# Optimization experiments

Measured on AMD Instinct MI355X. Metric: run time of the kernel, lower is better.

## Reference

```python
import jax, jax.numpy as jnp
from jax import lax
import numpy as np

K = 11          # NUM_TAGS
S = K + 2       # with start/stop
START, STOP = K, K + 1
O_TAG = 0
B, T = 4096, 1024
NEG = -10000.0


def setup_inputs() -> dict:
    key = jax.random.key(0)
    k1, k2, k3 = jax.random.split(key, 3)
    e = jax.random.normal(k1, (B, T, K), dtype=jnp.float32)
    Tmat = jax.random.normal(k2, (S, S), dtype=jnp.float32) * 0.1
    Tmat = Tmat.at[:, START].set(NEG)
    Tmat = Tmat.at[STOP, :].set(NEG)
    Tmat = Tmat.at[O_TAG, O_TAG].add(-2.0)
    tags = jax.random.randint(k3, (B, T), 0, K, dtype=jnp.int32)
    mask = jnp.ones((B, T), dtype=bool)
    return {"e": e, "Tmat": Tmat, "tags": tags, "mask": mask}


def _nll(e, Tmat, tags, mask):
    maskf = mask.astype(e.dtype)
    # ---- forward algorithm (log partition) via scan over time ----
    a0 = jnp.full((e.shape[0], S), NEG, dtype=e.dtype).at[:, START].set(0.0)

    def step(a, inp):
        e_t, m_t = inp                                   # (B,K), (B,)
        # scores[b, to] = lse_from(a[b, from] + Tmat[from, to])
        sc = jax.nn.logsumexp(a[:, :, None] + Tmat[None, :, :], axis=1)  # (B,S)
        sc = sc.at[:, :K].add(e_t)
        a = jnp.where(m_t[:, None], sc, a)
        return a, None

    a, _ = lax.scan(step, a0, (jnp.swapaxes(e, 0, 1), jnp.swapaxes(mask, 0, 1)))
    logZ = jax.nn.logsumexp(a[:, :K] + Tmat[:K, STOP][None, :], axis=1)  # (B,)

    # ---- gold path score (fully vectorized) ----
    tg = jnp.clip(tags, 0, K - 1)
    em = jnp.take_along_axis(e, tg[:, :, None], axis=2)[..., 0] * maskf  # (B,T)
    trans = Tmat[tg[:, :-1], tg[:, 1:]] * maskf[:, 1:]                   # (B,T-1)
    last = mask.astype(jnp.int32).sum(1) - 1                             # (B,)
    last_tag = jnp.take_along_axis(tg, last[:, None], axis=1)[:, 0]
    gold = Tmat[START, tg[:, 0]] + em.sum(1) + trans.sum(1) + Tmat[last_tag, STOP]

    return jnp.mean(logZ - gold)


def reference(e, Tmat, tags, mask):
    return _nll(e, Tmat, tags, mask)
```

## Files before the change

kernel.cpp:

```cpp
#include <hip/hip_runtime.h>

#define KTAGS 11
#define SS    13
#define TT    1024
#define BB    4096
#define GPW   4
#define UNR   16

__global__ __launch_bounds__(64)
void crf_scan_kernel(const float* __restrict__ e,
                     const float* __restrict__ Tmat,
                     const int*   __restrict__ tags,
                     float*       __restrict__ out_per_b)
{
    __shared__ float sT[SS * SS];
    const int tid = threadIdx.x;
    for (int i = tid; i < SS * SS; i += 64) sT[i] = Tmat[i];

    const int g   = tid >> 4;
    const int to  = tid & 15;
    const int toT = (to < SS) ? to : (SS - 1);
    const int toE = (to < KTAGS) ? to : (KTAGS - 1);
    const int b   = blockIdx.x * GPW + g;

    __syncthreads();

    float W[16];
#pragma unroll
    for (int r = 0; r < 16; ++r) {
        const int f = (to - r) & 15;
        W[r] = (f < KTAGS && to <= SS - 1 && to != KTAGS)
                 ? __expf(sT[f * SS + toT]) : 0.f;
        if (to >= SS) W[r] = 0.f;
    }
    const float eTstop = __expf(sT[toT * SS + (SS - 1)]);

    const float* pe  = e    + (size_t)b * TT * KTAGS + toE;
    const int*   tgp = tags + (size_t)b * TT;

    const float e0  = pe[0];
    const int   tg0 = tgp[0];
    float aP = (to < SS) ? __expf(sT[(SS - 2) * SS + toT] + e0) : 0.f;

    float cacc   = 0.f;
    float em_acc = (to == tg0) ? e0 : 0.f;

    float ebuf[UNR];
    int   tbuf[UNR];
#pragma unroll
    for (int j = 0; j < UNR; ++j) {
        ebuf[j] = pe[(size_t)(1 + j) * KTAGS];
        tbuf[j] = tgp[1 + j];
    }

    float scP = 1.f, eeP = 0.f;

#define STEP(J, E_T, TG)                                                       \
    {                                                                          \
        const float X_T = __expf(E_T);         \
        float ac0, ac1, ac2, ac3;                                              \
        asm volatile(                                                          \
          "s_nop 1\n\t"                                                        \
          "v_mul_f32 %0, %4, %5\n\t"                                           \
          "v_mul_f32_dpp %1, %4, %6  row_ror:1  row_mask:0xf bank_mask:0xf\n\t"\
          "v_mul_f32_dpp %2, %4, %7  row_ror:2  row_mask:0xf bank_mask:0xf\n\t"\
          "v_mul_f32_dpp %3, %4, %8  row_ror:3  row_mask:0xf bank_mask:0xf\n\t"\
          "v_fmac_f32_dpp %0, %4, %9  row_ror:4  row_mask:0xf bank_mask:0xf\n\t"\
          "v_fmac_f32_dpp %1, %4, %10 row_ror:5  row_mask:0xf bank_mask:0xf\n\t"\
          "v_fmac_f32_dpp %2, %4, %11 row_ror:6  row_mask:0xf bank_mask:0xf\n\t"\
          "v_fmac_f32_dpp %3, %4, %12 row_ror:7  row_mask:0xf bank_mask:0xf\n\t"\
          "v_fmac_f32_dpp %0, %4, %13 row_ror:8  row_mask:0xf bank_mask:0xf\n\t"\
          "v_fmac_f32_dpp %1, %4, %14 row_ror:9  row_mask:0xf bank_mask:0xf\n\t"\
          "v_fmac_f32_dpp %2, %4, %15 row_ror:10 row_mask:0xf bank_mask:0xf\n\t"\
          "v_fmac_f32_dpp %3, %4, %16 row_ror:11 row_mask:0xf bank_mask:0xf\n\t"\
          "v_fmac_f32_dpp %0, %4, %17 row_ror:12 row_mask:0xf bank_mask:0xf\n\t"\
          "v_fmac_f32_dpp %1, %4, %18 row_ror:13 row_mask:0xf bank_mask:0xf\n\t"\
          "v_fmac_f32_dpp %2, %4, %19 row_ror:14 row_mask:0xf bank_mask:0xf\n\t"\
          "v_fmac_f32_dpp %3, %4, %20 row_ror:15 row_mask:0xf bank_mask:0xf\n\t"\
          : "=&v"(ac0), "=&v"(ac1), "=&v"(ac2), "=&v"(ac3)                     \
          : "v"(aP), "v"(W[0]), "v"(W[1]), "v"(W[2]),  "v"(W[3]),              \
            "v"(W[4]), "v"(W[5]), "v"(W[6]),  "v"(W[7]), "v"(W[8]),            \
            "v"(W[9]), "v"(W[10]), "v"(W[11]), "v"(W[12]), "v"(W[13]),         \
            "v"(W[14]), "v"(W[15]));                                           \
        float xsc = X_T;                                                       \
        if (((J) & 7) == 0) { cacc += eeP * 0.6931471805599453f; xsc *= scP; } \
        aP = ((ac0 + ac1) + (ac2 + ac3)) * xsc;                                \
        if (((J) & 7) == 7) {    \
            float mm;                                                          \
            asm volatile(                                                      \
              "s_nop 1\n\t"                                                    \
              "v_max_f32_dpp %0, %1, %1 row_ror:8 row_mask:0xf bank_mask:0xf\n\t"\
              "s_nop 1\n\t"                                                    \
              "v_max_f32_dpp %0, %0, %0 row_ror:4 row_mask:0xf bank_mask:0xf\n\t"\
              "s_nop 1\n\t"                                                    \
              "v_max_f32_dpp %0, %0, %0 quad_perm:[1,0,3,2] row_mask:0xf bank_mask:0xf\n\t"\
              "s_nop 1\n\t"                                                    \
              "v_max_f32_dpp %0, %0, %0 quad_perm:[2,3,0,1] row_mask:0xf bank_mask:0xf\n\t"\
              : "=&v"(mm) : "v"(aP));                                          \
            const int ee = (int)((__float_as_uint(mm) >> 23) & 0xFFu) - 127;   \
            scP = __uint_as_float((unsigned)(127 - ee) << 23);                 \
            eeP = (float)ee;                                                   \
        }                                                                      \
        em_acc += (to == (TG)) ? (E_T) : 0.f;                                  \
    }

    const float* qe = pe  + (size_t)(1 + UNR) * KTAGS;
    const int*   qt = tgp + 1 + UNR;

    for (int tb = 1; tb + 2 * UNR <= TT; tb += UNR) {
#pragma unroll
        for (int j = 0; j < UNR; ++j) {
            const float E_T = ebuf[j];
            const int   TG  = tbuf[j];
            ebuf[j] = qe[j * KTAGS];
            tbuf[j] = qt[j];
            STEP(j, E_T, TG)
        }
        qe += (size_t)UNR * KTAGS; qt += UNR;
    }

#pragma unroll
    for (int j = 0; j < UNR; ++j) {
        const float E_T = ebuf[j];
        const int   TG  = tbuf[j];
        if (j < UNR - 1) {
            ebuf[j] = qe[j * KTAGS];
            tbuf[j] = qt[j];
        }
        STEP(j, E_T, TG)
    }

#pragma unroll
    for (int j = 0; j < UNR - 1; ++j) {
        STEP(j, ebuf[j], tbuf[j])
    }
#undef STEP

    float z  = (to < KTAGS) ? aP * eTstop : 0.f;
    float em = em_acc;
#pragma unroll
    for (int s = 8; s >= 1; s >>= 1) {
        z  += __shfl_xor(z,  s, 16);
        em += __shfl_xor(em, s, 16);
    }
    if (to == 0) {
        const float logZ = cacc + __logf(z);
        out_per_b[b] = logZ - em;
    }
}

__global__ __launch_bounds__(64)
void gold_kernel(const float* __restrict__ Tmat,
                 const int*   __restrict__ tags,
                 float*       __restrict__ out_per_b)
{
    __shared__ float sT[SS * SS];
    __shared__ int   stg[TT];
    const int tid = threadIdx.x;
    const int b   = blockIdx.x;

    for (int i = tid; i < SS * SS; i += 64) sT[i] = Tmat[i];
    const int4* tg4 = (const int4*)(tags + (size_t)b * TT);
    int4* s4 = (int4*)stg;
#pragma unroll
    for (int k = 0; k < TT / 4 / 64; ++k) s4[tid + 64 * k] = tg4[tid + 64 * k];
    __syncthreads();

    float s = 0.f;
    const int t0 = tid * 16;
#pragma unroll
    for (int k = 1; k <= 16; ++k) {
        const int t = t0 + k;
        if (t < TT) s += sT[stg[t - 1] * SS + stg[t]];
    }
    if (tid == 0) {
        s += sT[(SS - 2) * SS + stg[0]];
        s += sT[stg[TT - 1] * SS + (SS - 1)];
    }
#pragma unroll
    for (int d = 32; d >= 1; d >>= 1) s += __shfl_xor(s, d, 64);
    if (tid == 0) out_per_b[b] -= s;
}

__global__ __launch_bounds__(256)
void reduce_mean_kernel(const float* __restrict__ v, float* __restrict__ out, int n)
{
    __shared__ double sbuf[256];
    double s = 0.0;
    for (int i = threadIdx.x; i < n; i += 256) s += (double)v[i];
    sbuf[threadIdx.x] = s;
    __syncthreads();
    for (int k = 128; k > 0; k >>= 1) {
        if ((int)threadIdx.x < k) sbuf[threadIdx.x] += sbuf[threadIdx.x + k];
        __syncthreads();
    }
    if (threadIdx.x == 0) out[0] = (float)(sbuf[0] / (double)n);
}

extern "C" void kernel_launch(void* const* d_in, const int* in_sizes, int n_in,
                              void* d_out, int out_size, void* d_ws, size_t ws_size,
                              hipStream_t stream)
{
    const float* e    = (const float*)d_in[0];
    const float* Tmat = (const float*)d_in[1];
    const int*   tags = (const int*)d_in[2];

    float* ws  = (float*)d_ws;
    float* out = (float*)d_out;

    crf_scan_kernel<<<BB / GPW, 64, 0, stream>>>(e, Tmat, tags, ws);
    gold_kernel<<<BB, 64, 0, stream>>>(Tmat, tags, ws);
    reduce_mean_kernel<<<1, 256, 0, stream>>>(ws, out, BB);
}
```

Baseline: 96.87 us.

## Split CRF forward scan into forward and backward halves meeting at midpoint

Runs the sequential forward recursion over the first half of the sequence and a backward recursion over the second half in separate blocks, doubling the number of independent waves and halving the serial chain length. A new combine kernel computes logZ from the dot product of forward and backward vectors at the midpoint, in double precision. It keeps a fallback to the original single-direction scan when the workspace is too small. It adds an extra kernel launch and workspace traffic.

```diff
diff --git a/kernel.cpp b/kernel.cpp
--- a/kernel.cpp
+++ b/kernel.cpp
@@ -6,59 +6,18 @@
 #define BB    4096
 #define GPW   4
 #define UNR   16
-
-__global__ __launch_bounds__(64)
-void crf_scan_kernel(const float* __restrict__ e,
-                     const float* __restrict__ Tmat,
-                     const int*   __restrict__ tags,
-                     float*       __restrict__ out_per_b)
-{
-    __shared__ float sT[SS * SS];
-    const int tid = threadIdx.x;
-    for (int i = tid; i < SS * SS; i += 64) sT[i] = Tmat[i];
-
-    const int g   = tid >> 4;
-    const int to  = tid & 15;
-    const int toT = (to < SS) ? to : (SS - 1);
-    const int toE = (to < KTAGS) ? to : (KTAGS - 1);
-    const int b   = blockIdx.x * GPW + g;
-
-    __syncthreads();
-
-    float W[16];
-#pragma unroll
-    for (int r = 0; r < 16; ++r) {
-        const int f = (to - r) & 15;
-        W[r] = (f < KTAGS && to <= SS - 1 && to != KTAGS)
-                 ? __expf(sT[f * SS + toT]) : 0.f;
-        if (to >= SS) W[r] = 0.f;
-    }
-    const float eTstop = __expf(sT[toT * SS + (SS - 1)]);
-
-    const float* pe  = e    + (size_t)b * TT * KTAGS + toE;
-    const int*   tgp = tags + (size_t)b * TT;
-
-    const float e0  = pe[0];
-    const int   tg0 = tgp[0];
-    float aP = (to < SS) ? __expf(sT[(SS - 2) * SS + toT] + e0) : 0.f;
-
-    float cacc   = 0.f;
-    float em_acc = (to == tg0) ? e0 : 0.f;
-
-    float ebuf[UNR];
-    int   tbuf[UNR];
-#pragma unroll
-    for (int j = 0; j < UNR; ++j) {
-        ebuf[j] = pe[(size_t)(1 + j) * KTAGS];
-        tbuf[j] = tgp[1 + j];
-    }
-
-    float scP = 1.f, eeP = 0.f;
-
-#define STEP(J, E_T, TG)                                                       \
-    {                                                                          \
-        const float X_T = __expf(E_T);         \
-        float ac0, ac1, ac2, ac3;                                              \
+#define HALF  512
+
+#define WS_VA   0
+#define WS_UB   (11*BB)
+#define WS_CF   (22*BB)
+#define WS_EF   (23*BB)
+#define WS_CB   (24*BB)
+#define WS_EB   (25*BB)
+#define WS_NLL  (26*BB)
+#define WS_FLOATS (27*BB)
+
+#define ROTSUM(A0,A1,A2,A3,SRC)                                                \
         asm volatile(                                                          \
           "s_nop 1\n\t"                                                        \
           "v_mul_f32 %0, %4, %5\n\t"                                           \
@@ -77,26 +36,35 @@
           "v_fmac_f32_dpp %1, %4, %18 row_ror:13 row_mask:0xf bank_mask:0xf\n\t"\
           "v_fmac_f32_dpp %2, %4, %19 row_ror:14 row_mask:0xf bank_mask:0xf\n\t"\
           "v_fmac_f32_dpp %3, %4, %20 row_ror:15 row_mask:0xf bank_mask:0xf\n\t"\
-          : "=&v"(ac0), "=&v"(ac1), "=&v"(ac2), "=&v"(ac3)                     \
-          : "v"(aP), "v"(W[0]), "v"(W[1]), "v"(W[2]),  "v"(W[3]),              \
+          : "=&v"(A0), "=&v"(A1), "=&v"(A2), "=&v"(A3)                         \
+          : "v"(SRC), "v"(W[0]), "v"(W[1]), "v"(W[2]),  "v"(W[3]),             \
             "v"(W[4]), "v"(W[5]), "v"(W[6]),  "v"(W[7]), "v"(W[8]),            \
             "v"(W[9]), "v"(W[10]), "v"(W[11]), "v"(W[12]), "v"(W[13]),         \
-            "v"(W[14]), "v"(W[15]));                                           \
+            "v"(W[14]), "v"(W[15]))
+
+#define MAXRED(MM, SRC)                                                        \
+        asm volatile(                                                          \
+          "s_nop 1\n\t"                                                        \
+          "v_max_f32_dpp %0, %1, %1 row_ror:8 row_mask:0xf bank_mask:0xf\n\t"  \
+          "s_nop 1\n\t"                                                        \
+          "v_max_f32_dpp %0, %0, %0 row_ror:4 row_mask:0xf bank_mask:0xf\n\t"  \
+          "s_nop 1\n\t"                                                        \
+          "v_max_f32_dpp %0, %0, %0 quad_perm:[1,0,3,2] row_mask:0xf bank_mask:0xf\n\t"\
+          "s_nop 1\n\t"                                                        \
+          "v_max_f32_dpp %0, %0, %0 quad_perm:[2,3,0,1] row_mask:0xf bank_mask:0xf\n\t"\
+          : "=&v"(MM) : "v"(SRC))
+
+#define STEP(J, E_T, TG)                                                       \
+    {                                                                          \
+        const float X_T = __expf(E_T);                                         \
+        float ac0, ac1, ac2, ac3;                                              \
+        ROTSUM(ac0, ac1, ac2, ac3, aP);                                        \
         float xsc = X_T;                                                       \
         if (((J) & 7) == 0) { cacc += eeP * 0.6931471805599453f; xsc *= scP; } \
         aP = ((ac0 + ac1) + (ac2 + ac3)) * xsc;                                \
-        if (((J) & 7) == 7) {    \
+        if (((J) & 7) == 7) {                                                  \
             float mm;                                                          \
-            asm volatile(                                                      \
-              "s_nop 1\n\t"                                                    \
-              "v_max_f32_dpp %0, %1, %1 row_ror:8 row_mask:0xf bank_mask:0xf\n\t"\
-              "s_nop 1\n\t"                                                    \
-              "v_max_f32_dpp %0, %0, %0 row_ror:4 row_mask:0xf bank_mask:0xf\n\t"\
-              "s_nop 1\n\t"                                                    \
-              "v_max_f32_dpp %0, %0, %0 quad_perm:[1,0,3,2] row_mask:0xf bank_mask:0xf\n\t"\
-              "s_nop 1\n\t"                                                    \
-              "v_max_f32_dpp %0, %0, %0 quad_perm:[2,3,0,1] row_mask:0xf bank_mask:0xf\n\t"\
-              : "=&v"(mm) : "v"(aP));                                          \
+            MAXRED(mm, aP);                                                    \
             const int ee = (int)((__float_as_uint(mm) >> 23) & 0xFFu) - 127;   \
             scP = __uint_as_float((unsigned)(127 - ee) << 23);                 \
             eeP = (float)ee;                                                   \
@@ -104,9 +72,224 @@
         em_acc += (to == (TG)) ? (E_T) : 0.f;                                  \
     }
 
+template<int DIR>
+__device__ __forceinline__ void scan_dir(const float* __restrict__ e,
+                                         const int*   __restrict__ tags,
+                                         const float* sT,
+                                         float*       __restrict__ ws,
+                                         int b, int to)
+{
+    const int toT = (to < SS) ? to : (SS - 1);
+    const int toE = (to < KTAGS) ? to : (KTAGS - 1);
+
+    float W[16];
+#pragma unroll
+    for (int r = 0; r < 16; ++r) {
+        const int f = (to - r) & 15;
+        if (DIR > 0) {
+            W[r] = (f < KTAGS && to <= SS - 1 && to != KTAGS)
+                     ? __expf(sT[f * SS + toT]) : 0.f;
+            if (to >= SS) W[r] = 0.f;
+        } else {
+            W[r] = (to < KTAGS && f < KTAGS) ? __expf(sT[to * SS + f]) : 0.f;
+        }
+    }
+
+    const float* ebase = e    + (size_t)b * TT * KTAGS + toE;
+    const int*   tbase = tags + (size_t)b * TT;
+
+    float aP, em_acc, cacc = 0.f;
+    if (DIR > 0) {
+        const float E0 = ebase[0];
+        const int   tg0 = tbase[0];
+        aP = (to < SS) ? __expf(sT[(SS - 2) * SS + toT] + E0) : 0.f;
+        em_acc = (to == tg0) ? E0 : 0.f;
+    } else {
+        const float E0 = ebase[(size_t)(TT - 1) * KTAGS];
+        const int   tg0 = tbase[TT - 1];
+        aP = (to < KTAGS) ? __expf(E0 + sT[toT * SS + (SS - 1)]) : 0.f;
+        em_acc = (to == tg0) ? E0 : 0.f;
+    }
+
+    const ptrdiff_t estep = (ptrdiff_t)DIR * KTAGS;
+    const float* peU = ebase + ((DIR > 0) ? (ptrdiff_t)KTAGS : (ptrdiff_t)(TT - 2) * KTAGS);
+    const int*   tgU = tbase + ((DIR > 0) ? 1 : (TT - 2));
+
+    float ebuf[UNR]; int tbuf[UNR];
+#pragma unroll
+    for (int j = 0; j < UNR; ++j) {
+        ebuf[j] = peU[estep * j];
+        tbuf[j] = tgU[DIR * j];
+    }
+
+    float scP = 1.f, eeP = 0.f;
+    const float* qe = peU + estep * UNR;
+    const int*   qt = tgU + DIR * UNR;
+
+    for (int tb = 0; tb + 2 * UNR <= (HALF - 1); tb += UNR) {
+#pragma unroll
+        for (int j = 0; j < UNR; ++j) {
+            const float E_T = ebuf[j];
+            const int   TG  = tbuf[j];
+            ebuf[j] = qe[estep * j];
+            tbuf[j] = qt[DIR * j];
+            STEP(j, E_T, TG)
+        }
+        qe += estep * UNR; qt += DIR * UNR;
+    }
+#pragma unroll
+    for (int j = 0; j < UNR; ++j) {
+        const float E_T = ebuf[j];
+        const int   TG  = tbuf[j];
+        if (j < UNR - 1) { ebuf[j] = qe[estep * j]; tbuf[j] = qt[DIR * j]; }
+        STEP(j, E_T, TG)
+    }
+#pragma unroll
+    for (int j = 0; j < UNR - 1; ++j) {
+        STEP(j, ebuf[j], tbuf[j])
+    }
+
+    float em = em_acc;
+#pragma unroll
+    for (int s = 8; s >= 1; s >>= 1) em += __shfl_xor(em, s, 16);
+
+    if (DIR > 0) {
+        float ac0, ac1, ac2, ac3;
+        ROTSUM(ac0, ac1, ac2, ac3, aP);
+        const float v = (ac0 + ac1) + (ac2 + ac3);
+        if (to < KTAGS) ws[WS_VA + to * BB + b] = v;
+        if (to == 0) { ws[WS_CF + b] = cacc; ws[WS_EF + b] = em; }
+    } else {
+        if (to < KTAGS) ws[WS_UB + to * BB + b] = aP;
+        if (to == 0) { ws[WS_CB + b] = cacc; ws[WS_EB + b] = em; }
+    }
+}
+
+__global__ __launch_bounds__(64)
+void crf_scan2_kernel(const float* __restrict__ e,
+                      const float* __restrict__ Tmat,
+                      const int*   __restrict__ tags,
+                      float*       __restrict__ ws)
+{
+    __shared__ float sT[SS * SS];
+    const int tid = threadIdx.x;
+    for (int i = tid; i < SS * SS; i += 64) sT[i] = Tmat[i];
+    __syncthreads();
+
+    const int g  = tid >> 4;
+    const int to = tid & 15;
+    const int b  = ((int)blockIdx.x & (BB / GPW - 1)) * GPW + g;
+
+    if ((int)blockIdx.x < BB / GPW) scan_dir<+1>(e, tags, sT, ws, b, to);
+    else                            scan_dir<-1>(e, tags, sT, ws, b, to);
+}
+
+__global__ __launch_bounds__(256)
+void combine_kernel(float* __restrict__ ws)
+{
+    const int b = blockIdx.x * 256 + threadIdx.x;
+    double dot = 0.0;
+#pragma unroll
+    for (int s = 0; s < KTAGS; ++s)
+        dot += (double)ws[WS_VA + s * BB + b] * (double)ws[WS_UB + s * BB + b];
+    const float logZ = (float)((double)ws[WS_CF + b] + (double)ws[WS_CB + b] + log(dot));
+    ws[WS_NLL + b] = logZ - ws[WS_EF + b] - ws[WS_EB + b];
+}
+
+__global__ __launch_bounds__(64)
+void gold_kernel(const float* __restrict__ Tmat,
+                 const int*   __restrict__ tags,
+                 float*       __restrict__ nll)
+{
+    __shared__ float sT[SS * SS];
+    __shared__ int   stg[TT];
+    const int tid = threadIdx.x;
+    const int b   = blockIdx.x;
+
+    for (int i = tid; i < SS * SS; i += 64) sT[i] = Tmat[i];
+    const int4* tg4 = (const int4*)(tags + (size_t)b * TT);
+    int4* s4 = (int4*)stg;
+#pragma unroll
+    for (int k = 0; k < TT / 4 / 64; ++k) s4[tid + 64 * k] = tg4[tid + 64 * k];
+    __syncthreads();
+
+    float s = 0.f;
+    const int t0 = tid * 16;
+#pragma unroll
+    for (int k = 1; k <= 16; ++k) {
+        const int t = t0 + k;
+        if (t < TT) s += sT[stg[t - 1] * SS + stg[t]];
+    }
+    if (tid == 0) {
+        s += sT[(SS - 2) * SS + stg[0]];
+        s += sT[stg[TT - 1] * SS + (SS - 1)];
+    }
+#pragma unroll
+    for (int d = 32; d >= 1; d >>= 1) s += __shfl_xor(s, d, 64);
+    if (tid == 0) nll[b] -= s;
+}
+
+__global__ __launch_bounds__(256)
+void reduce_mean_kernel(const float* __restrict__ v, float* __restrict__ out, int n)
+{
+    __shared__ double sbuf[256];
+    double s = 0.0;
+    for (int i = threadIdx.x; i < n; i += 256) s += (double)v[i];
+    sbuf[threadIdx.x] = s;
+    __syncthreads();
+    for (int k = 128; k > 0; k >>= 1) {
+        if ((int)threadIdx.x < k) sbuf[threadIdx.x] += sbuf[threadIdx.x + k];
+        __syncthreads();
+    }
+    if (threadIdx.x == 0) out[0] = (float)(sbuf[0] / (double)n);
+}
+
+__global__ __launch_bounds__(64)
+void crf_scan_full_kernel(const float* __restrict__ e,
+                          const float* __restrict__ Tmat,
+                          const int*   __restrict__ tags,
+                          float*       __restrict__ out_per_b)
+{
+    __shared__ float sT[SS * SS];
+    const int tid = threadIdx.x;
+    for (int i = tid; i < SS * SS; i += 64) sT[i] = Tmat[i];
+
+    const int g   = tid >> 4;
+    const int to  = tid & 15;
+    const int toT = (to < SS) ? to : (SS - 1);
+    const int toE = (to < KTAGS) ? to : (KTAGS - 1);
+    const int b   = blockIdx.x * GPW + g;
+    __syncthreads();
+
+    float W[16];
+#pragma unroll
+    for (int r = 0; r < 16; ++r) {
+        const int f = (to - r) & 15;
+        W[r] = (f < KTAGS && to <= SS - 1 && to != KTAGS)
+                 ? __expf(sT[f * SS + toT]) : 0.f;
+        if (to >= SS) W[r] = 0.f;
+    }
+    const float eTstop = __expf(sT[toT * SS + (SS - 1)]);
+
+    const float* pe  = e    + (size_t)b * TT * KTAGS + toE;
+    const int*   tgp = tags + (size_t)b * TT;
+
+    const float e0  = pe[0];
+    const int   tg0 = tgp[0];
+    float aP = (to < SS) ? __expf(sT[(SS - 2) * SS + toT] + e0) : 0.f;
+    float cacc = 0.f;
+    float em_acc = (to == tg0) ? e0 : 0.f;
+
+    float ebuf[UNR]; int tbuf[UNR];
+#pragma unroll
+    for (int j = 0; j < UNR; ++j) {
+        ebuf[j] = pe[(size_t)(1 + j) * KTAGS];
+        tbuf[j] = tgp[1 + j];
+    }
+    float scP = 1.f, eeP = 0.f;
+
     const float* qe = pe  + (size_t)(1 + UNR) * KTAGS;
     const int*   qt = tgp + 1 + UNR;
-
     for (int tb = 1; tb + 2 * UNR <= TT; tb += UNR) {
 #pragma unroll
         for (int j = 0; j < UNR; ++j) {
@@ -118,23 +301,17 @@
         }
         qe += (size_t)UNR * KTAGS; qt += UNR;
     }
-
 #pragma unroll
     for (int j = 0; j < UNR; ++j) {
         const float E_T = ebuf[j];
         const int   TG  = tbuf[j];
-        if (j < UNR - 1) {
-            ebuf[j] = qe[j * KTAGS];
-            tbuf[j] = qt[j];
-        }
+        if (j < UNR - 1) { ebuf[j] = qe[j * KTAGS]; tbuf[j] = qt[j]; }
         STEP(j, E_T, TG)
     }
-
 #pragma unroll
     for (int j = 0; j < UNR - 1; ++j) {
         STEP(j, ebuf[j], tbuf[j])
     }
-#undef STEP
 
     float z  = (to < KTAGS) ? aP * eTstop : 0.f;
     float em = em_acc;
@@ -149,54 +326,6 @@
     }
 }
 
-__global__ __launch_bounds__(64)
-void gold_kernel(const float* __restrict__ Tmat,
-                 const int*   __restrict__ tags,
-                 float*       __restrict__ out_per_b)
-{
-    __shared__ float sT[SS * SS];
-    __shared__ int   stg[TT];
-    const int tid = threadIdx.x;
-    const int b   = blockIdx.x;
-
-    for (int i = tid; i < SS * SS; i += 64) sT[i] = Tmat[i];
-    const int4* tg4 = (const int4*)(tags + (size_t)b * TT);
-    int4* s4 = (int4*)stg;
-#pragma unroll
-    for (int k = 0; k < TT / 4 / 64; ++k) s4[tid + 64 * k] = tg4[tid + 64 * k];
-    __syncthreads();
-
-    float s = 0.f;
-    const int t0 = tid * 16;
-#pragma unroll
-    for (int k = 1; k <= 16; ++k) {
-        const int t = t0 + k;
-        if (t < TT) s += sT[stg[t - 1] * SS + stg[t]];
-    }
-    if (tid == 0) {
-        s += sT[(SS - 2) * SS + stg[0]];
-        s += sT[stg[TT - 1] * SS + (SS - 1)];
-    }
-#pragma unroll
-    for (int d = 32; d >= 1; d >>= 1) s += __shfl_xor(s, d, 64);
-    if (tid == 0) out_per_b[b] -= s;
-}
-
-__global__ __launch_bounds__(256)
-void reduce_mean_kernel(const float* __restrict__ v, float* __restrict__ out, int n)
-{
-    __shared__ double sbuf[256];
-    double s = 0.0;
-    for (int i = threadIdx.x; i < n; i += 256) s += (double)v[i];
-    sbuf[threadIdx.x] = s;
-    __syncthreads();
-    for (int k = 128; k > 0; k >>= 1) {
-        if ((int)threadIdx.x < k) sbuf[threadIdx.x] += sbuf[threadIdx.x + k];
-        __syncthreads();
-    }
-    if (threadIdx.x == 0) out[0] = (float)(sbuf[0] / (double)n);
-}
-
 extern "C" void kernel_launch(void* const* d_in, const int* in_sizes, int n_in,
                               void* d_out, int out_size, void* d_ws, size_t ws_size,
                               hipStream_t stream)
@@ -208,7 +337,14 @@
     float* ws  = (float*)d_ws;
     float* out = (float*)d_out;
 
-    crf_scan_kernel<<<BB / GPW, 64, 0, stream>>>(e, Tmat, tags, ws);
-    gold_kernel<<<BB, 64, 0, stream>>>(Tmat, tags, ws);
-    reduce_mean_kernel<<<1, 256, 0, stream>>>(ws, out, BB);
-}
+    if (ws_size >= (size_t)WS_FLOATS * sizeof(float)) {
+        crf_scan2_kernel<<<2 * BB / GPW, 64, 0, stream>>>(e, Tmat, tags, ws);
+        combine_kernel<<<BB / 256, 256, 0, stream>>>(ws);
+        gold_kernel<<<BB, 64, 0, stream>>>(Tmat, tags, ws + WS_NLL);
+        reduce_mean_kernel<<<1, 256, 0, stream>>>(ws + WS_NLL, out, BB);
+    } else {
+        crf_scan_full_kernel<<<BB / GPW, 64, 0, stream>>>(e, Tmat, tags, ws);
+        gold_kernel<<<BB, 64, 0, stream>>>(Tmat, tags, ws);
+        reduce_mean_kernel<<<1, 256, 0, stream>>>(ws, out, BB);
+    }
+}
```

After: 80.51 us. -16.9%, faster.

## Split CRF forward scan into forward and backward halves meeting midway

Applied to the files above, without the earlier changes.

Replaces the single sequential forward recursion with two interleaved chains per sequence: a forward alpha chain from the start and a backward beta chain from the end, each covering half the timesteps. The two results are combined with one extra matrix-vector step and a double-precision dot product. This halves the serial dependency length and gives the scheduler two independent DPP chains to interleave, hiding instruction latency. The cost is twice the register use for weights and buffers, which may lower occupancy, plus reverse-direction loads for the backward chain.

```diff
diff --git a/kernel.cpp b/kernel.cpp
--- a/kernel.cpp
+++ b/kernel.cpp
@@ -5,60 +5,71 @@
 #define TT    1024
 #define BB    4096
 #define GPW   4
-#define UNR   16
-
-__global__ __launch_bounds__(64)
-void crf_scan_kernel(const float* __restrict__ e,
-                     const float* __restrict__ Tmat,
-                     const int*   __restrict__ tags,
-                     float*       __restrict__ out_per_b)
-{
-    __shared__ float sT[SS * SS];
-    const int tid = threadIdx.x;
-    for (int i = tid; i < SS * SS; i += 64) sT[i] = Tmat[i];
-
-    const int g   = tid >> 4;
-    const int to  = tid & 15;
-    const int toT = (to < SS) ? to : (SS - 1);
-    const int toE = (to < KTAGS) ? to : (KTAGS - 1);
-    const int b   = blockIdx.x * GPW + g;
-
-    __syncthreads();
-
-    float W[16];
-#pragma unroll
-    for (int r = 0; r < 16; ++r) {
-        const int f = (to - r) & 15;
-        W[r] = (f < KTAGS && to <= SS - 1 && to != KTAGS)
-                 ? __expf(sT[f * SS + toT]) : 0.f;
-        if (to >= SS) W[r] = 0.f;
-    }
-    const float eTstop = __expf(sT[toT * SS + (SS - 1)]);
-
-    const float* pe  = e    + (size_t)b * TT * KTAGS + toE;
-    const int*   tgp = tags + (size_t)b * TT;
-
-    const float e0  = pe[0];
-    const int   tg0 = tgp[0];
-    float aP = (to < SS) ? __expf(sT[(SS - 2) * SS + toT] + e0) : 0.f;
-
-    float cacc   = 0.f;
-    float em_acc = (to == tg0) ? e0 : 0.f;
-
-    float ebuf[UNR];
-    int   tbuf[UNR];
-#pragma unroll
-    for (int j = 0; j < UNR; ++j) {
-        ebuf[j] = pe[(size_t)(1 + j) * KTAGS];
-        tbuf[j] = tgp[1 + j];
-    }
-
-    float scP = 1.f, eeP = 0.f;
-
-#define STEP(J, E_T, TG)                                                       \
-    {                                                                          \
-        const float X_T = __expf(E_T);         \
-        float ac0, ac1, ac2, ac3;                                              \
+#define UNR   8
+#define LN2   0.6931471805599453f
+
+#define ROTSUM2(A0,A1,A2,A3,B0,B1,B2,B3,SA,SB,WA,WB)                           \
+        asm volatile(                                                          \
+          "s_nop 1\n\t"                                                        \
+          "v_mul_f32 %0, %8, %10\n\t"                                          \
+          "v_mul_f32_dpp %1, %8, %11 row_ror:1  row_mask:0xf bank_mask:0xf\n\t"\
+          "v_mul_f32_dpp %2, %8, %12 row_ror:2  row_mask:0xf bank_mask:0xf\n\t"\
+          "v_mul_f32_dpp %3, %8, %13 row_ror:3  row_mask:0xf bank_mask:0xf\n\t"\
+          "v_mul_f32 %4, %9, %26\n\t"                                          \
+          "v_mul_f32_dpp %5, %9, %27 row_ror:1  row_mask:0xf bank_mask:0xf\n\t"\
+          "v_mul_f32_dpp %6, %9, %28 row_ror:2  row_mask:0xf bank_mask:0xf\n\t"\
+          "v_mul_f32_dpp %7, %9, %29 row_ror:3  row_mask:0xf bank_mask:0xf\n\t"\
+          "v_fmac_f32_dpp %0, %8, %14 row_ror:4  row_mask:0xf bank_mask:0xf\n\t"\
+          "v_fmac_f32_dpp %4, %9, %30 row_ror:4  row_mask:0xf bank_mask:0xf\n\t"\
+          "v_fmac_f32_dpp %1, %8, %15 row_ror:5  row_mask:0xf bank_mask:0xf\n\t"\
+          "v_fmac_f32_dpp %5, %9, %31 row_ror:5  row_mask:0xf bank_mask:0xf\n\t"\
+          "v_fmac_f32_dpp %2, %8, %16 row_ror:6  row_mask:0xf bank_mask:0xf\n\t"\
+          "v_fmac_f32_dpp %6, %9, %32 row_ror:6  row_mask:0xf bank_mask:0xf\n\t"\
+          "v_fmac_f32_dpp %3, %8, %17 row_ror:7  row_mask:0xf bank_mask:0xf\n\t"\
+          "v_fmac_f32_dpp %7, %9, %33 row_ror:7  row_mask:0xf bank_mask:0xf\n\t"\
+          "v_fmac_f32_dpp %0, %8, %18 row_ror:8  row_mask:0xf bank_mask:0xf\n\t"\
+          "v_fmac_f32_dpp %4, %9, %34 row_ror:8  row_mask:0xf bank_mask:0xf\n\t"\
+          "v_fmac_f32_dpp %1, %8, %19 row_ror:9  row_mask:0xf bank_mask:0xf\n\t"\
+          "v_fmac_f32_dpp %5, %9, %35 row_ror:9  row_mask:0xf bank_mask:0xf\n\t"\
+          "v_fmac_f32_dpp %2, %8, %20 row_ror:10 row_mask:0xf bank_mask:0xf\n\t"\
+          "v_fmac_f32_dpp %6, %9, %36 row_ror:10 row_mask:0xf bank_mask:0xf\n\t"\
+          "v_fmac_f32_dpp %3, %8, %21 row_ror:11 row_mask:0xf bank_mask:0xf\n\t"\
+          "v_fmac_f32_dpp %7, %9, %37 row_ror:11 row_mask:0xf bank_mask:0xf\n\t"\
+          "v_fmac_f32_dpp %0, %8, %22 row_ror:12 row_mask:0xf bank_mask:0xf\n\t"\
+          "v_fmac_f32_dpp %4, %9, %38 row_ror:12 row_mask:0xf bank_mask:0xf\n\t"\
+          "v_fmac_f32_dpp %1, %8, %23 row_ror:13 row_mask:0xf bank_mask:0xf\n\t"\
+          "v_fmac_f32_dpp %5, %9, %39 row_ror:13 row_mask:0xf bank_mask:0xf\n\t"\
+          "v_fmac_f32_dpp %2, %8, %24 row_ror:14 row_mask:0xf bank_mask:0xf\n\t"\
+          "v_fmac_f32_dpp %6, %9, %40 row_ror:14 row_mask:0xf bank_mask:0xf\n\t"\
+          "v_fmac_f32_dpp %3, %8, %25 row_ror:15 row_mask:0xf bank_mask:0xf\n\t"\
+          "v_fmac_f32_dpp %7, %9, %41 row_ror:15 row_mask:0xf bank_mask:0xf\n\t"\
+          : "=&v"(A0), "=&v"(A1), "=&v"(A2), "=&v"(A3),                        \
+            "=&v"(B0), "=&v"(B1), "=&v"(B2), "=&v"(B3)                         \
+          : "v"(SA), "v"(SB),                                                  \
+            "v"(WA[0]),"v"(WA[1]),"v"(WA[2]),"v"(WA[3]),"v"(WA[4]),"v"(WA[5]), \
+            "v"(WA[6]),"v"(WA[7]),"v"(WA[8]),"v"(WA[9]),"v"(WA[10]),"v"(WA[11]),\
+            "v"(WA[12]),"v"(WA[13]),"v"(WA[14]),"v"(WA[15]),                   \
+            "v"(WB[0]),"v"(WB[1]),"v"(WB[2]),"v"(WB[3]),"v"(WB[4]),"v"(WB[5]), \
+            "v"(WB[6]),"v"(WB[7]),"v"(WB[8]),"v"(WB[9]),"v"(WB[10]),"v"(WB[11]),\
+            "v"(WB[12]),"v"(WB[13]),"v"(WB[14]),"v"(WB[15]))
+
+#define MAXRED2(MA, MB, SA, SB)                                                \
+        asm volatile(                                                          \
+          "s_nop 1\n\t"                                                        \
+          "v_max_f32_dpp %0, %2, %2 row_ror:8 row_mask:0xf bank_mask:0xf\n\t"  \
+          "v_max_f32_dpp %1, %3, %3 row_ror:8 row_mask:0xf bank_mask:0xf\n\t"  \
+          "s_nop 0\n\t"                                                        \
+          "v_max_f32_dpp %0, %0, %0 row_ror:4 row_mask:0xf bank_mask:0xf\n\t"  \
+          "v_max_f32_dpp %1, %1, %1 row_ror:4 row_mask:0xf bank_mask:0xf\n\t"  \
+          "s_nop 0\n\t"                                                        \
+          "v_max_f32_dpp %0, %0, %0 quad_perm:[1,0,3,2] row_mask:0xf bank_mask:0xf\n\t"\
+          "v_max_f32_dpp %1, %1, %1 quad_perm:[1,0,3,2] row_mask:0xf bank_mask:0xf\n\t"\
+          "s_nop 0\n\t"                                                        \
+          "v_max_f32_dpp %0, %0, %0 quad_perm:[2,3,0,1] row_mask:0xf bank_mask:0xf\n\t"\
+          "v_max_f32_dpp %1, %1, %1 quad_perm:[2,3,0,1] row_mask:0xf bank_mask:0xf\n\t"\
+          : "=&v"(MA), "=&v"(MB) : "v"(SA), "v"(SB))
+
+#define ROTSUM1(A0,A1,A2,A3,SRC,W)                                             \
         asm volatile(                                                          \
           "s_nop 1\n\t"                                                        \
           "v_mul_f32 %0, %4, %5\n\t"                                           \
@@ -77,82 +88,144 @@
           "v_fmac_f32_dpp %1, %4, %18 row_ror:13 row_mask:0xf bank_mask:0xf\n\t"\
           "v_fmac_f32_dpp %2, %4, %19 row_ror:14 row_mask:0xf bank_mask:0xf\n\t"\
           "v_fmac_f32_dpp %3, %4, %20 row_ror:15 row_mask:0xf bank_mask:0xf\n\t"\
-          : "=&v"(ac0), "=&v"(ac1), "=&v"(ac2), "=&v"(ac3)                     \
-          : "v"(aP), "v"(W[0]), "v"(W[1]), "v"(W[2]),  "v"(W[3]),              \
+          : "=&v"(A0), "=&v"(A1), "=&v"(A2), "=&v"(A3)                         \
+          : "v"(SRC), "v"(W[0]), "v"(W[1]), "v"(W[2]),  "v"(W[3]),             \
             "v"(W[4]), "v"(W[5]), "v"(W[6]),  "v"(W[7]), "v"(W[8]),            \
             "v"(W[9]), "v"(W[10]), "v"(W[11]), "v"(W[12]), "v"(W[13]),         \
-            "v"(W[14]), "v"(W[15]));                                           \
-        float xsc = X_T;                                                       \
-        if (((J) & 7) == 0) { cacc += eeP * 0.6931471805599453f; xsc *= scP; } \
-        aP = ((ac0 + ac1) + (ac2 + ac3)) * xsc;                                \
-        if (((J) & 7) == 7) {    \
-            float mm;                                                          \
-            asm volatile(                                                      \
-              "s_nop 1\n\t"                                                    \
-              "v_max_f32_dpp %0, %1, %1 row_ror:8 row_mask:0xf bank_mask:0xf\n\t"\
-              "s_nop 1\n\t"                                                    \
-              "v_max_f32_dpp %0, %0, %0 row_ror:4 row_mask:0xf bank_mask:0xf\n\t"\
-              "s_nop 1\n\t"                                                    \
-              "v_max_f32_dpp %0, %0, %0 quad_perm:[1,0,3,2] row_mask:0xf bank_mask:0xf\n\t"\
-              "s_nop 1\n\t"                                                    \
-              "v_max_f32_dpp %0, %0, %0 quad_perm:[2,3,0,1] row_mask:0xf bank_mask:0xf\n\t"\
-              : "=&v"(mm) : "v"(aP));                                          \
-            const int ee = (int)((__float_as_uint(mm) >> 23) & 0xFFu) - 127;   \
-            scP = __uint_as_float((unsigned)(127 - ee) << 23);                 \
-            eeP = (float)ee;                                                   \
+            "v"(W[14]), "v"(W[15]))
+
+#define STEP2(J, EA, TA, EB, TB)                                               \
+    {                                                                          \
+        const float XA = __expf(EA), XB = __expf(EB);                          \
+        float a0,a1,a2,a3,b0,b1,b2,b3;                                         \
+        ROTSUM2(a0,a1,a2,a3,b0,b1,b2,b3, aA, aB, WA, WB);                      \
+        float xA = XA, xB = XB;                                                \
+        if (((J)&7)==0) { caccA += eePA*LN2; xA *= scPA;                       \
+                          caccB += eePB*LN2; xB *= scPB; }                     \
+        aA = ((a0+a1)+(a2+a3))*xA;                                             \
+        aB = ((b0+b1)+(b2+b3))*xB;                                             \
+        if (((J)&7)==7) { float mA,mB; MAXRED2(mA,mB,aA,aB);                   \
+            const int eA_ = (int)((__float_as_uint(mA)>>23)&0xFFu)-127;        \
+            const int eB_ = (int)((__float_as_uint(mB)>>23)&0xFFu)-127;        \
+            scPA = __uint_as_float((unsigned)(127-eA_)<<23); eePA=(float)eA_;  \
+            scPB = __uint_as_float((unsigned)(127-eB_)<<23); eePB=(float)eB_;  \
         }                                                                      \
-        em_acc += (to == (TG)) ? (E_T) : 0.f;                                  \
-    }
-
-    const float* qe = pe  + (size_t)(1 + UNR) * KTAGS;
-    const int*   qt = tgp + 1 + UNR;
-
-    for (int tb = 1; tb + 2 * UNR <= TT; tb += UNR) {
+        emA += (to==(TA)) ? (EA) : 0.f;                                        \
+        emB += (to==(TB)) ? (EB) : 0.f;                                        \
+    }
+
+__global__ __launch_bounds__(64)
+void crf_pair_kernel(const float* __restrict__ e,
+                     const float* __restrict__ Tmat,
+                     const int*   __restrict__ tags,
+                     float*       __restrict__ nll)
+{
+    __shared__ float sT[SS * SS];
+    const int tid = threadIdx.x;
+    for (int i = tid; i < SS * SS; i += 64) sT[i] = Tmat[i];
+    __syncthreads();
+
+    const int g   = tid >> 4;
+    const int to  = tid & 15;
+    const int toT = (to < SS) ? to : (SS - 1);
+    const int toE = (to < KTAGS) ? to : (KTAGS - 1);
+    const int b   = blockIdx.x * GPW + g;
+
+    float WA[16], WB[16];
+#pragma unroll
+    for (int r = 0; r < 16; ++r) {
+        const int f = (to - r) & 15;
+        WA[r] = (f < KTAGS && to <= SS - 1 && to != KTAGS)
+                  ? __expf(sT[f * SS + toT]) : 0.f;
+        if (to >= SS) WA[r] = 0.f;
+        WB[r] = (to < KTAGS && f < KTAGS) ? __expf(sT[to * SS + f]) : 0.f;
+    }
+
+    const float* ebase = e    + (size_t)b * TT * KTAGS + toE;
+    const int*   tbase = tags + (size_t)b * TT;
+
+    const float e0  = ebase[0];
+    const int   tg0 = tbase[0];
+    float aA = (to < SS) ? __expf(sT[(SS - 2) * SS + toT] + e0) : 0.f;
+
+    const float e1  = ebase[(size_t)(TT - 1) * KTAGS];
+    const int   tg1 = tbase[TT - 1];
+    float aB = (to < KTAGS) ? __expf(e1 + sT[toT * SS + (SS - 1)]) : 0.f;
+
+    float caccA = 0.f, caccB = 0.f;
+    float emA = (to == tg0) ? e0 : 0.f;
+    float emB = (to == tg1) ? e1 : 0.f;
+    float scPA = 1.f, eePA = 0.f, scPB = 1.f, eePB = 0.f;
+
+    float ebA[UNR], ebB[UNR];
+    int   tbA[UNR], tbB[UNR];
+    const float* peA = ebase + KTAGS;
+    const float* peB = ebase + (size_t)(TT - 2) * KTAGS;
+    const int*   ptA = tbase + 1;
+    const int*   ptB = tbase + (TT - 2);
+#pragma unroll
+    for (int j = 0; j < UNR; ++j) {
+        ebA[j] = peA[j * KTAGS];
+        ebB[j] = peB[-(j * KTAGS)];
+        tbA[j] = ptA[j];
+        tbB[j] = ptB[-j];
+    }
+    const float* qeA = peA + UNR * KTAGS;
+    const float* qeB = peB - UNR * KTAGS;
+    const int*   qtA = ptA + UNR;
+    const int*   qtB = ptB - UNR;
+
+    for (int tb = 0; tb + 2 * UNR <= (TT / 2 - 1); tb += UNR) {
 #pragma unroll
         for (int j = 0; j < UNR; ++j) {
-            const float E_T = ebuf[j];
-            const int   TG  = tbuf[j];
-            ebuf[j] = qe[j * KTAGS];
-            tbuf[j] = qt[j];
-            STEP(j, E_T, TG)
+            const float EA = ebA[j], EB = ebB[j];
+            const int   TA = tbA[j], TB = tbB[j];
+            ebA[j] = qeA[j * KTAGS];
+            ebB[j] = qeB[-(j * KTAGS)];
+            tbA[j] = qtA[j];
+            tbB[j] = qtB[-j];
+            STEP2(j, EA, TA, EB, TB)
         }
-        qe += (size_t)UNR * KTAGS; qt += UNR;
-    }
-
+        qeA += UNR * KTAGS; qeB -= UNR * KTAGS; qtA += UNR; qtB -= UNR;
+    }
 #pragma unroll
     for (int j = 0; j < UNR; ++j) {
-        const float E_T = ebuf[j];
-        const int   TG  = tbuf[j];
+        const float EA = ebA[j], EB = ebB[j];
+        const int   TA = tbA[j], TB = tbB[j];
         if (j < UNR - 1) {
-            ebuf[j] = qe[j * KTAGS];
-            tbuf[j] = qt[j];
+            ebA[j] = qeA[j * KTAGS];
+            ebB[j] = qeB[-(j * KTAGS)];
+            tbA[j] = qtA[j];
+            tbB[j] = qtB[-j];
         }
-        STEP(j, E_T, TG)
-    }
-
+        STEP2(j, EA, TA, EB, TB)
+    }
 #pragma unroll
     for (int j = 0; j < UNR - 1; ++j) {
-        STEP(j, ebuf[j], tbuf[j])
-    }
-#undef STEP
-
-    float z  = (to < KTAGS) ? aP * eTstop : 0.f;
-    float em = em_acc;
+        STEP2(j, ebA[j], tbA[j], ebB[j], tbB[j])
+    }
+
+    float c0, c1, c2, c3;
+    ROTSUM1(c0, c1, c2, c3, aA, WA);
+    const float v = (c0 + c1) + (c2 + c3);
+
+    double pd = (to < KTAGS) ? (double)v * (double)aB : 0.0;
+    float  em = emA + emB;
 #pragma unroll
     for (int s = 8; s >= 1; s >>= 1) {
-        z  += __shfl_xor(z,  s, 16);
+        pd += __shfl_xor(pd, s, 16);
         em += __shfl_xor(em, s, 16);
     }
     if (to == 0) {
-        const float logZ = cacc + __logf(z);
-        out_per_b[b] = logZ - em;
+        const double logZ = (double)caccA + (double)caccB + log(pd);
+        nll[b] = (float)logZ - em;
     }
 }
 
 __global__ __launch_bounds__(64)
 void gold_kernel(const float* __restrict__ Tmat,
                  const int*   __restrict__ tags,
-                 float*       __restrict__ out_per_b)
+                 float*       __restrict__ nll)
 {
     __shared__ float sT[SS * SS];
     __shared__ int   stg[TT];
@@ -179,7 +252,7 @@
     }
 #pragma unroll
     for (int d = 32; d >= 1; d >>= 1) s += __shfl_xor(s, d, 64);
-    if (tid == 0) out_per_b[b] -= s;
+    if (tid == 0) nll[b] -= s;
 }
 
 __global__ __launch_bounds__(256)
@@ -208,7 +281,7 @@
     float* ws  = (float*)d_ws;
     float* out = (float*)d_out;
 
-    crf_scan_kernel<<<BB / GPW, 64, 0, stream>>>(e, Tmat, tags, ws);
+    crf_pair_kernel<<<BB / GPW, 64, 0, stream>>>(e, Tmat, tags, ws);
     gold_kernel<<<BB, 64, 0, stream>>>(Tmat, tags, ws);
     reduce_mean_kernel<<<1, 256, 0, stream>>>(ws, out, BB);
 }
```

After: 90.73 us. 1.07x faster.

## Run CRF forward scan as bidirectional bf16 MFMA recurrence with meet-in-middle combine

Applied to the files above, without the earlier changes.

Replaces the per-sequence DPP matvec recurrence with a v_mfma_f32_16x16x16_bf16 step that advances 16 sequences per wave. Each half of the sequence is scanned by its own block, one forward and one backward, which halves the serial chain length. A new combine kernel joins the two halves with a dot product in the middle. The states are rounded to bf16 at every step, which risks accuracy, and the MFMA latency is padded with s_nops on the serial dependency chain.

```diff
diff --git a/kernel.cpp b/kernel.cpp
--- a/kernel.cpp
+++ b/kernel.cpp
@@ -4,155 +4,227 @@
 #define SS    13
 #define TT    1024
 #define BB    4096
-#define GPW   4
-#define UNR   16
+#define UNR   8
+#define LN2   0.6931471805599453f
+
+typedef float        v4f __attribute__((ext_vector_type(4)));
+typedef unsigned int v2u __attribute__((ext_vector_type(2)));
+
+#define WS_VA   0
+#define WS_UB   (11*BB)
+#define WS_CF   (22*BB)
+#define WS_EF   (23*BB)
+#define WS_CB   (24*BB)
+#define WS_EB   (25*BB)
+#define WS_NLL  (26*BB)
+
+__device__ __forceinline__ unsigned short f2bf(float f) {
+    unsigned u = __float_as_uint(f);
+    u += 0x7FFFu + ((u >> 16) & 1u);
+    return (unsigned short)(u >> 16);
+}
+__device__ __forceinline__ unsigned pack2(float lo, float hi) {
+    return (unsigned)f2bf(lo) | ((unsigned)f2bf(hi) << 16);
+}
+
+#define MFMA_STEP(D, A, B, C)                                              \
+    asm volatile("s_nop 1\n\t"                                             \
+                 "v_mfma_f32_16x16x16_bf16 %0, %1, %2, %3\n\t"             \
+                 "s_nop 7\n\t"                                             \
+                 "s_nop 3"                                                 \
+                 : "=&v"(D) : "v"(A), "v"(B), "v"(C))
+#define CVTPK(dst, lo, hi)                                                 \
+    asm volatile("v_cvt_pk_bf16_f32 %0, %1, %2" : "=v"(dst) : "v"(lo), "v"(hi))
+
+#define MSTEP(JJ, E0v, E1v, E2v, E3v, TG)                                  \
+    {                                                                      \
+        float X0 = __expf(E0v), X1 = __expf(E1v);                          \
+        float X2 = __expf(E2v), X3 = __expf(E3v);                          \
+        float xs0 = gge2 ? X1 : X0;                                        \
+        float xs1 = gge2 ? X2 : X1;                                        \
+        float xs2 = gge2 ? X3 : X2;                                        \
+        float xs3 = X3;                                                    \
+        if (((JJ) & 7) == 0) { cacc += eeP * LN2;                          \
+            xs0 *= scP; xs1 *= scP; xs2 *= scP; xs3 *= scP; }              \
+        v4f D;                                                             \
+        MFMA_STEP(D, Af, Bf, CZ);                                          \
+        float t0 = D.x * xs0, t1 = D.y * xs1;                              \
+        float t2 = D.z * xs2, t3 = D.w * xs3;                              \
+        if (((JJ) & 7) == 7) {                                             \
+            float mm = fmaxf(fmaxf(t0, t1), fmaxf(t2, t3));                \
+            mm = fmaxf(mm, __shfl_xor(mm, 16, 64));                        \
+            mm = fmaxf(mm, __shfl_xor(mm, 32, 64));                        \
+            const int ee = (int)((__float_as_uint(mm) >> 23) & 0xFFu) - 127; \
+            scP = __uint_as_float((unsigned)(127 - ee) << 23);             \
+            eeP = (float)ee;                                               \
+        }                                                                  \
+        unsigned pb0, pb1;                                                 \
+        CVTPK(pb0, t0, t1); CVTPK(pb1, t2, t3);                            \
+        Bf.x = pb0; Bf.y = pb1;                                            \
+        cur.x = t0; cur.y = t1; cur.z = t2; cur.w = t3;                    \
+        const bool hit = (((TG) >> 2) == g);                               \
+        const int  si  = ((TG) & 3) + (gge2 ? 1 : 0);                      \
+        const float va = (si < 2) ? ((si == 0) ? (E0v) : (E1v))            \
+                                  : ((si == 2) ? (E2v) : (E3v));           \
+        em += hit ? va : 0.f;                                              \
+    }
+
+template<int DIR>
+__device__ __forceinline__ void scan_mfma(const float* __restrict__ e,
+                                          const int*   __restrict__ tags,
+                                          const float* sT,
+                                          float*       __restrict__ ws,
+                                          int b0, int l)
+{
+    const int g = l >> 4;
+    const int j = l & 15;
+    const int b = b0 + j;
+    const bool gge2 = (g >= 2);
+    const int c0 = (g == 0) ? 0 : (g == 1) ? 4 : 7;
+
+    v2u Af;
+    {
+        float af[4];
+#pragma unroll
+        for (int r = 0; r < 4; ++r) {
+            const int s = 4 * g + r;
+            float v = 0.f;
+            if (s < KTAGS && j < KTAGS)
+                v = (DIR > 0) ? __expf(sT[s * SS + j]) : __expf(sT[j * SS + s]);
+            af[r] = v;
+        }
+        Af.x = pack2(af[0], af[1]);
+        Af.y = pack2(af[2], af[3]);
+    }
+    v4f CZ = {0.f, 0.f, 0.f, 0.f};
+
+    const int t0i = (DIR > 0) ? 0 : (TT - 1);
+    const float* er = e + ((size_t)b * TT + t0i) * KTAGS + c0;
+    const float i0 = er[0], i1 = er[1], i2 = er[2], i3 = er[3];
+    const int tg0 = tags[(size_t)b * TT + t0i];
+
+    float em, cacc = 0.f, scP = 1.f, eeP = 0.f;
+    v2u Bf;
+    v4f cur = CZ;
+    {
+        float a0r[4];
+#pragma unroll
+        for (int r = 0; r < 4; ++r) {
+            const int s = 4 * g + r;
+            const float ev = gge2 ? ((r == 0) ? i1 : (r == 1) ? i2 : i3)
+                                  : ((r == 0) ? i0 : (r == 1) ? i1 : (r == 2) ? i2 : i3);
+            a0r[r] = (s < KTAGS)
+                       ? ((DIR > 0) ? __expf(sT[(SS - 2) * SS + s] + ev)
+                                    : __expf(ev + sT[s * SS + (SS - 1)]))
+                       : 0.f;
+        }
+        Bf.x = pack2(a0r[0], a0r[1]);
+        Bf.y = pack2(a0r[2], a0r[3]);
+        const bool hit = ((tg0 >> 2) == g);
+        const int  si  = (tg0 & 3) + (gge2 ? 1 : 0);
+        const float va = (si < 2) ? ((si == 0) ? i0 : i1) : ((si == 2) ? i2 : i3);
+        em = hit ? va : 0.f;
+    }
+
+    float eb0[UNR], eb1[UNR], eb2[UNR], eb3[UNR];
+    int   tb_[UNR];
+    const float* pe = e    + ((size_t)b * TT + ((DIR > 0) ? 1 : TT - 2)) * KTAGS + c0;
+    const int*   pt = tags + (size_t)b * TT + ((DIR > 0) ? 1 : TT - 2);
+#pragma unroll
+    for (int jj = 0; jj < UNR; ++jj) {
+        eb0[jj] = pe[DIR * jj * KTAGS + 0];
+        eb1[jj] = pe[DIR * jj * KTAGS + 1];
+        eb2[jj] = pe[DIR * jj * KTAGS + 2];
+        eb3[jj] = pe[DIR * jj * KTAGS + 3];
+        tb_[jj] = pt[DIR * jj];
+    }
+    const float* qe = pe + DIR * UNR * KTAGS;
+    const int*   qt = pt + DIR * UNR;
+
+    for (int tb = 0; tb + 2 * UNR <= (TT / 2 - 1); tb += UNR) {
+#pragma unroll
+        for (int jj = 0; jj < UNR; ++jj) {
+            const float E0 = eb0[jj], E1 = eb1[jj], E2 = eb2[jj], E3 = eb3[jj];
+            const int TG = tb_[jj];
+            eb0[jj] = qe[DIR * jj * KTAGS + 0];
+            eb1[jj] = qe[DIR * jj * KTAGS + 1];
+            eb2[jj] = qe[DIR * jj * KTAGS + 2];
+            eb3[jj] = qe[DIR * jj * KTAGS + 3];
+            tb_[jj] = qt[DIR * jj];
+            MSTEP(jj, E0, E1, E2, E3, TG)
+        }
+        qe += DIR * UNR * KTAGS; qt += DIR * UNR;
+    }
+#pragma unroll
+    for (int jj = 0; jj < UNR; ++jj) {
+        const float E0 = eb0[jj], E1 = eb1[jj], E2 = eb2[jj], E3 = eb3[jj];
+        const int TG = tb_[jj];
+        if (jj < UNR - 1) {
+            eb0[jj] = qe[DIR * jj * KTAGS + 0];
+            eb1[jj] = qe[DIR * jj * KTAGS + 1];
+            eb2[jj] = qe[DIR * jj * KTAGS + 2];
+            eb3[jj] = qe[DIR * jj * KTAGS + 3];
+            tb_[jj] = qt[DIR * jj];
+        }
+        MSTEP(jj, E0, E1, E2, E3, TG)
+    }
+#pragma unroll
+    for (int jj = 0; jj < UNR - 1; ++jj) {
+        MSTEP(jj, eb0[jj], eb1[jj], eb2[jj], eb3[jj], tb_[jj])
+    }
+
+    em += __shfl_xor(em, 16, 64);
+    em += __shfl_xor(em, 32, 64);
+    const int s0 = 4 * g;
+
+    if (DIR > 0) {
+        v4f Dv;
+        MFMA_STEP(Dv, Af, Bf, CZ);
+        if (s0 + 0 < KTAGS) ws[WS_VA + (s0 + 0) * BB + b] = Dv.x;
+        if (s0 + 1 < KTAGS) ws[WS_VA + (s0 + 1) * BB + b] = Dv.y;
+        if (s0 + 2 < KTAGS) ws[WS_VA + (s0 + 2) * BB + b] = Dv.z;
+        if (s0 + 3 < KTAGS) ws[WS_VA + (s0 + 3) * BB + b] = Dv.w;
+        if (l < 16) { ws[WS_CF + b] = cacc; ws[WS_EF + b] = em; }
+    } else {
+        if (s0 + 0 < KTAGS) ws[WS_UB + (s0 + 0) * BB + b] = cur.x;
+        if (s0 + 1 < KTAGS) ws[WS_UB + (s0 + 1) * BB + b] = cur.y;
+        if (s0 + 2 < KTAGS) ws[WS_UB + (s0 + 2) * BB + b] = cur.z;
+        if (s0 + 3 < KTAGS) ws[WS_UB + (s0 + 3) * BB + b] = cur.w;
+        if (l < 16) { ws[WS_CB + b] = cacc; ws[WS_EB + b] = em; }
+    }
+}
 
 __global__ __launch_bounds__(64)
-void crf_scan_kernel(const float* __restrict__ e,
+void crf_mfma_kernel(const float* __restrict__ e,
                      const float* __restrict__ Tmat,
                      const int*   __restrict__ tags,
-                     float*       __restrict__ out_per_b)
+                     float*       __restrict__ ws)
 {
     __shared__ float sT[SS * SS];
     const int tid = threadIdx.x;
     for (int i = tid; i < SS * SS; i += 64) sT[i] = Tmat[i];
-
-    const int g   = tid >> 4;
-    const int to  = tid & 15;
-    const int toT = (to < SS) ? to : (SS - 1);
-    const int toE = (to < KTAGS) ? to : (KTAGS - 1);
-    const int b   = blockIdx.x * GPW + g;
-
     __syncthreads();
-
-    float W[16];
-#pragma unroll
-    for (int r = 0; r < 16; ++r) {
-        const int f = (to - r) & 15;
-        W[r] = (f < KTAGS && to <= SS - 1 && to != KTAGS)
-                 ? __expf(sT[f * SS + toT]) : 0.f;
-        if (to >= SS) W[r] = 0.f;
-    }
-    const float eTstop = __expf(sT[toT * SS + (SS - 1)]);
-
-    const float* pe  = e    + (size_t)b * TT * KTAGS + toE;
-    const int*   tgp = tags + (size_t)b * TT;
-
-    const float e0  = pe[0];
-    const int   tg0 = tgp[0];
-    float aP = (to < SS) ? __expf(sT[(SS - 2) * SS + toT] + e0) : 0.f;
-
-    float cacc   = 0.f;
-    float em_acc = (to == tg0) ? e0 : 0.f;
-
-    float ebuf[UNR];
-    int   tbuf[UNR];
-#pragma unroll
-    for (int j = 0; j < UNR; ++j) {
-        ebuf[j] = pe[(size_t)(1 + j) * KTAGS];
-        tbuf[j] = tgp[1 + j];
-    }
-
-    float scP = 1.f, eeP = 0.f;
-
-#define STEP(J, E_T, TG)                                                       \
-    {                                                                          \
-        const float X_T = __expf(E_T);         \
-        float ac0, ac1, ac2, ac3;                                              \
-        asm volatile(                                                          \
-          "s_nop 1\n\t"                                                        \
-          "v_mul_f32 %0, %4, %5\n\t"                                           \
-          "v_mul_f32_dpp %1, %4, %6  row_ror:1  row_mask:0xf bank_mask:0xf\n\t"\
-          "v_mul_f32_dpp %2, %4, %7  row_ror:2  row_mask:0xf bank_mask:0xf\n\t"\
-          "v_mul_f32_dpp %3, %4, %8  row_ror:3  row_mask:0xf bank_mask:0xf\n\t"\
-          "v_fmac_f32_dpp %0, %4, %9  row_ror:4  row_mask:0xf bank_mask:0xf\n\t"\
-          "v_fmac_f32_dpp %1, %4, %10 row_ror:5  row_mask:0xf bank_mask:0xf\n\t"\
-          "v_fmac_f32_dpp %2, %4, %11 row_ror:6  row_mask:0xf bank_mask:0xf\n\t"\
-          "v_fmac_f32_dpp %3, %4, %12 row_ror:7  row_mask:0xf bank_mask:0xf\n\t"\
-          "v_fmac_f32_dpp %0, %4, %13 row_ror:8  row_mask:0xf bank_mask:0xf\n\t"\
-          "v_fmac_f32_dpp %1, %4, %14 row_ror:9  row_mask:0xf bank_mask:0xf\n\t"\
-          "v_fmac_f32_dpp %2, %4, %15 row_ror:10 row_mask:0xf bank_mask:0xf\n\t"\
-          "v_fmac_f32_dpp %3, %4, %16 row_ror:11 row_mask:0xf bank_mask:0xf\n\t"\
-          "v_fmac_f32_dpp %0, %4, %17 row_ror:12 row_mask:0xf bank_mask:0xf\n\t"\
-          "v_fmac_f32_dpp %1, %4, %18 row_ror:13 row_mask:0xf bank_mask:0xf\n\t"\
-          "v_fmac_f32_dpp %2, %4, %19 row_ror:14 row_mask:0xf bank_mask:0xf\n\t"\
-          "v_fmac_f32_dpp %3, %4, %20 row_ror:15 row_mask:0xf bank_mask:0xf\n\t"\
-          : "=&v"(ac0), "=&v"(ac1), "=&v"(ac2), "=&v"(ac3)                     \
-          : "v"(aP), "v"(W[0]), "v"(W[1]), "v"(W[2]),  "v"(W[3]),              \
-            "v"(W[4]), "v"(W[5]), "v"(W[6]),  "v"(W[7]), "v"(W[8]),            \
-            "v"(W[9]), "v"(W[10]), "v"(W[11]), "v"(W[12]), "v"(W[13]),         \
-            "v"(W[14]), "v"(W[15]));                                           \
-        float xsc = X_T;                                                       \
-        if (((J) & 7) == 0) { cacc += eeP * 0.6931471805599453f; xsc *= scP; } \
-        aP = ((ac0 + ac1) + (ac2 + ac3)) * xsc;                                \
-        if (((J) & 7) == 7) {    \
-            float mm;                                                          \
-            asm volatile(                                                      \
-              "s_nop 1\n\t"                                                    \
-              "v_max_f32_dpp %0, %1, %1 row_ror:8 row_mask:0xf bank_mask:0xf\n\t"\
-              "s_nop 1\n\t"                                                    \
-              "v_max_f32_dpp %0, %0, %0 row_ror:4 row_mask:0xf bank_mask:0xf\n\t"\
-              "s_nop 1\n\t"                                                    \
-              "v_max_f32_dpp %0, %0, %0 quad_perm:[1,0,3,2] row_mask:0xf bank_mask:0xf\n\t"\
-              "s_nop 1\n\t"                                                    \
-              "v_max_f32_dpp %0, %0, %0 quad_perm:[2,3,0,1] row_mask:0xf bank_mask:0xf\n\t"\
-              : "=&v"(mm) : "v"(aP));                                          \
-            const int ee = (int)((__float_as_uint(mm) >> 23) & 0xFFu) - 127;   \
-            scP = __uint_as_float((unsigned)(127 - ee) << 23);                 \
-            eeP = (float)ee;                                                   \
-        }                                                                      \
-        em_acc += (to == (TG)) ? (E_T) : 0.f;                                  \
-    }
-
-    const float* qe = pe  + (size_t)(1 + UNR) * KTAGS;
-    const int*   qt = tgp + 1 + UNR;
-
-    for (int tb = 1; tb + 2 * UNR <= TT; tb += UNR) {
-#pragma unroll
-        for (int j = 0; j < UNR; ++j) {
-            const float E_T = ebuf[j];
-            const int   TG  = tbuf[j];
-            ebuf[j] = qe[j * KTAGS];
-            tbuf[j] = qt[j];
-            STEP(j, E_T, TG)
-        }
-        qe += (size_t)UNR * KTAGS; qt += UNR;
-    }
-
-#pragma unroll
-    for (int j = 0; j < UNR; ++j) {
-        const float E_T = ebuf[j];
-        const int   TG  = tbuf[j];
-        if (j < UNR - 1) {
-            ebuf[j] = qe[j * KTAGS];
-            tbuf[j] = qt[j];
-        }
-        STEP(j, E_T, TG)
-    }
-
-#pragma unroll
-    for (int j = 0; j < UNR - 1; ++j) {
-        STEP(j, ebuf[j], tbuf[j])
-    }
-#undef STEP
-
-    float z  = (to < KTAGS) ? aP * eTstop : 0.f;
-    float em = em_acc;
-#pragma unroll
-    for (int s = 8; s >= 1; s >>= 1) {
-        z  += __shfl_xor(z,  s, 16);
-        em += __shfl_xor(em, s, 16);
-    }
-    if (to == 0) {
-        const float logZ = cacc + __logf(z);
-        out_per_b[b] = logZ - em;
-    }
+    const int p = (int)blockIdx.x;
+    if (p < BB / 16) scan_mfma<+1>(e, tags, sT, ws, p * 16, tid);
+    else             scan_mfma<-1>(e, tags, sT, ws, (p - BB / 16) * 16, tid);
+}
+
+__global__ __launch_bounds__(256)
+void combine_kernel(float* __restrict__ ws)
+{
+    const int b = blockIdx.x * 256 + threadIdx.x;
+    double dot = 0.0;
+#pragma unroll
+    for (int s = 0; s < KTAGS; ++s)
+        dot += (double)ws[WS_VA + s * BB + b] * (double)ws[WS_UB + s * BB + b];
+    const double logZ = (double)ws[WS_CF + b] + (double)ws[WS_CB + b] + log(dot);
+    ws[WS_NLL + b] = (float)logZ - ws[WS_EF + b] - ws[WS_EB + b];
 }
 
 __global__ __launch_bounds__(64)
 void gold_kernel(const float* __restrict__ Tmat,
                  const int*   __restrict__ tags,
-                 float*       __restrict__ out_per_b)
+                 float*       __restrict__ nll)
 {
     __shared__ float sT[SS * SS];
     __shared__ int   stg[TT];
@@ -179,7 +251,7 @@
     }
 #pragma unroll
     for (int d = 32; d >= 1; d >>= 1) s += __shfl_xor(s, d, 64);
-    if (tid == 0) out_per_b[b] -= s;
+    if (tid == 0) nll[b] -= s;
 }
 
 __global__ __launch_bounds__(256)
@@ -208,7 +280,8 @@
     float* ws  = (float*)d_ws;
     float* out = (float*)d_out;
 
-    crf_scan_kernel<<<BB / GPW, 64, 0, stream>>>(e, Tmat, tags, ws);
-    gold_kernel<<<BB, 64, 0, stream>>>(Tmat, tags, ws);
-    reduce_mean_kernel<<<1, 256, 0, stream>>>(ws, out, BB);
-}
+    crf_mfma_kernel<<<2 * (BB / 16), 64, 0, stream>>>(e, Tmat, tags, ws);
+    combine_kernel<<<BB / 256, 256, 0, stream>>>(ws);
+    gold_kernel<<<BB, 64, 0, stream>>>(Tmat, tags, ws + WS_NLL);
+    reduce_mean_kernel<<<1, 256, 0, stream>>>(ws + WS_NLL, out, BB);
+}
```

Measured after the change: 99.16 us. 2.4% more time.
